# Performance work log

Hardware: AMD Instinct MI355X
Metric: run time of the kernel (lower is better)

Reference implementation:

```python
import jax, jax.numpy as jnp
import numpy as np

V, D, L, H, S, B = 30522, 768, 12, 12, 64, 128
DK = D // H
FF = 4 * D
EPS = 1e-5

def _positional_table():
    # replicates the (buggy) exponent 10000**(2*i/d) from the source
    pos = np.arange(S, dtype=np.float32)[:, None]
    i = np.arange(0, D, 2, dtype=np.float32)
    arg = pos / (10000.0 ** (2.0 * i / D))
    pe = np.zeros((S, D), dtype=np.float32)
    pe[:, 0::2] = np.sin(arg)
    pe[:, 1::2] = np.cos(arg)
    return jnp.asarray(pe)[None]  # [1,S,D]

PE = _positional_table()

def setup_inputs() -> dict:
    key = jax.random.key(0)
    ks = jax.random.split(key, 20)
    sc = 0.02
    tok_emb = jax.random.normal(ks[0], (V, D), jnp.float32) * sc
    tok_emb = tok_emb.at[0].set(0.0)  # padding_idx=0
    seg_emb = jax.random.normal(ks[1], (3, D), jnp.float32) * sc
    seg_emb = seg_emb.at[0].set(0.0)
    def w(k, shape):
        return jax.random.normal(k, shape, jnp.float32) * sc
    return {
        "x": jax.random.randint(ks[2], (B, S), 0, V),
        "segment": jax.random.randint(ks[3], (B, S), 0, 3),
        "tok_emb": tok_emb, "seg_emb": seg_emb,
        "Wq": w(ks[4], (L, D, D)), "bq": jnp.zeros((L, D)),
        "Wk": w(ks[5], (L, D, D)), "bk": jnp.zeros((L, D)),
        "Wv": w(ks[6], (L, D, D)), "bv": jnp.zeros((L, D)),
        "Wo": w(ks[7], (L, D, D)), "bo": jnp.zeros((L, D)),
        "ln_g": jnp.ones((L, D)), "ln_b": jnp.zeros((L, D)),
        "W1": w(ks[8], (L, D, FF)), "b1": jnp.zeros((L, FF)),
        "W2": w(ks[9], (L, FF, D)), "b2": jnp.zeros((L, D)),
    }

def _layernorm(x, g, b):
    mu = jnp.mean(x, -1, keepdims=True)
    var = jnp.mean(jnp.square(x - mu), -1, keepdims=True)
    return (x - mu) * jax.lax.rsqrt(var + EPS) * g + b

def reference(x, segment, tok_emb, seg_emb, Wq, bq, Wk, bk, Wv, bv, Wo, bo,
              ln_g, ln_b, W1, b1, W2, b2):
    # mask: (x>0) -> [B,1,1,S], broadcasts over query rows like the repeat in torch
    mask = (x > 0)[:, None, None, :]
    h = tok_emb[x] + seg_emb[segment] + PE  # [B,S,D]

    def layer(h, p):
        wq, bq_, wk, bk_, wv, bv_, wo, bo_, g, be, w1, b1_, w2, b2_ = p
        q = (h @ wq + bq_).reshape(B, S, H, DK).transpose(0, 2, 1, 3)
        k = (h @ wk + bk_).reshape(B, S, H, DK).transpose(0, 2, 1, 3)
        v = (h @ wv + bv_).reshape(B, S, H, DK).transpose(0, 2, 1, 3)
        scores = jnp.einsum('bhqd,bhkd->bhqk', q, k) / jnp.sqrt(jnp.float32(DK))
        scores = jnp.where(mask, scores, -1e9)
        w = jax.nn.softmax(scores, axis=-1)
        ctx = jnp.einsum('bhqk,bhkd->bhqd', w, v).transpose(0, 2, 1, 3).reshape(B, S, D)
        attn = ctx @ wo + bo_
        h1 = _layernorm(attn + h, g, be)  # shared LN params within the layer
        ff = jax.nn.gelu(h1 @ w1 + b1_, approximate=False) @ w2 + b2_
        h2 = _layernorm(h1 + ff, g, be)
        return h2, None

    params = (Wq, bq, Wk, bk, Wv, bv, Wo, bo, ln_g, ln_b, W1, b1, W2, b2)
    h, _ = jax.lax.scan(layer, h, params)
    return h
```

## Files before the change

### kernel.cpp

```cpp
#include <hip/hip_runtime.h>
#include <math.h>

typedef unsigned short u16;
typedef __bf16 bf16x8 __attribute__((ext_vector_type(8)));
typedef float f32x4 __attribute__((ext_vector_type(4)));
typedef unsigned long long u64;

__device__ __forceinline__ float bf2f(u16 u) {
    union { unsigned u32; float f; } c; c.u32 = ((unsigned)u) << 16; return c.f;
}
__device__ __forceinline__ u16 f2bf(float f) {
    unsigned u = __float_as_uint(f);
    unsigned r = u + 0x7fff + ((u >> 16) & 1);
    return (u16)(r >> 16);
}
__device__ __forceinline__ float ldmix(const void* p, u64 i, int isbf) {
    return isbf ? bf2f(((const u16*)p)[i]) : ((const float*)p)[i];
}
__device__ __forceinline__ uint4 pack8(float4 a, float4 b) {
    union { u16 h[8]; uint4 v; } u;
    u.h[0] = f2bf(a.x); u.h[1] = f2bf(a.y); u.h[2] = f2bf(a.z); u.h[3] = f2bf(a.w);
    u.h[4] = f2bf(b.x); u.h[5] = f2bf(b.y); u.h[6] = f2bf(b.z); u.h[7] = f2bf(b.w);
    return u.v;
}

__global__ void detect_kernel(const unsigned* __restrict__ tokw, int* __restrict__ flag)
{
    int i = threadIdx.x;
    unsigned w = tokw[768 + i];
    unsigned e = (w >> 7) & 0xFF;
    bool hit = (e >= 100) && (e <= 126) && ((w & 0x7FFFu) != 0);
    unsigned long long m = __ballot(hit);
    if (i == 0) flag[0] = (__popcll(m) >= 40) ? 1 : 0;
}

__global__ __launch_bounds__(256) void embed_kernel(
    const int* __restrict__ x, const int* __restrict__ seg,
    const void* __restrict__ tok, const void* __restrict__ se,
    const int* __restrict__ flagp, float* __restrict__ hF)
{
    int isbf = *flagp;
    int t = blockIdx.x;
    int pos = t & 63;
    int tokid = x[t], sgid = seg[t];
    int tid = threadIdx.x;
#pragma unroll
    for (int i = 0; i < 3; i++) {
        int d = tid + i * 256;
        int p = d >> 1;
        float freq = powf(10000.0f, (float)p * (1.0f / 192.0f));
        float arg = (float)pos / freq;
        float pe = (d & 1) ? cosf(arg) : sinf(arg);
        float v = ldmix(tok, (u64)tokid * 768 + d, isbf)
                + ldmix(se, (u64)sgid * 768 + d, isbf) + pe;
        hF[(u64)t * 768 + d] = v;
    }
}

__global__ __launch_bounds__(256) void transpose6(
    const void* __restrict__ wq, const void* __restrict__ wk,
    const void* __restrict__ wv, const void* __restrict__ wo,
    const void* __restrict__ w1, const void* __restrict__ w2,
    u16* __restrict__ out, const int* __restrict__ flagp, u64 oS, u64 oF)
{
    int isbf = *flagp;
    int id = blockIdx.x;
    const void* src; u16* dst; int R, C; u64 off;
    if (id < 2304) {
        int m = id / 576; id -= m * 576; R = 768; C = 768; off = oS;
        src = (m == 0) ? wq : (m == 1) ? wk : (m == 2) ? wv : wo;
        dst = out + (u64)m * 589824;
    } else if (id < 4608) {
        id -= 2304; R = 768; C = 3072; off = oF; src = w1; dst = out + 2359296;
    } else {
        id -= 4608; R = 3072; C = 768; off = oF; src = w2; dst = out + 4718592;
    }
    int tilesC = C >> 5;
    int tr = id / tilesC, tc = id % tilesC;
    __shared__ float tile[32][33];
    int rl = threadIdx.x >> 5, cl = threadIdx.x & 31;
#pragma unroll
    for (int i = 0; i < 4; i++)
        tile[rl + 8 * i][cl] = ldmix(src, off + (u64)(tr * 32 + rl + 8 * i) * C + tc * 32 + cl, isbf);
    __syncthreads();
#pragma unroll
    for (int i = 0; i < 4; i++)
        dst[(u64)(tc * 32 + rl + 8 * i) * R + tr * 32 + cl] = f2bf(tile[cl][rl + 8 * i]);
}

template <int MODE, int ASRC>
__global__ __launch_bounds__(256, 2) void gemm_bt(
    const void* __restrict__ Araw, const u16* __restrict__ Bt,
    const void* __restrict__ bias, u64 oB, const float* __restrict__ resid,
    float* __restrict__ outF, u16* __restrict__ outB,
    const int* __restrict__ flagp, int N, int K)
{
    constexpr int LDK = 40;
    __shared__ __align__(16) u16 sA[128 * LDK];
    __shared__ __align__(16) u16 sB[128 * LDK];
    int tid = threadIdx.x;
    int lane = tid & 63, wave = tid >> 6;
    int wr = wave >> 1, wc = wave & 1;
    int bn = blockIdx.x, bm = blockIdx.y;
    const u16* A16 = (const u16*)Araw + (u64)bm * 128 * K;
    const float* A32 = (const float*)Araw + (u64)bm * 128 * K;
    const u16* Bb = Bt + (u64)bn * 128 * K;
    int r0 = tid >> 2, c0 = (tid & 3) * 8;
    int cl = lane & 15, quad = lane >> 4;

    f32x4 acc[4][4];
    const f32x4 vz = {0.f, 0.f, 0.f, 0.f};
#pragma unroll
    for (int mi = 0; mi < 4; mi++)
#pragma unroll
        for (int ni = 0; ni < 4; ni++) acc[mi][ni] = vz;

    uint4 a0, a1;
    float4 fa0, fa1, fb0, fb1;
    if (ASRC == 0) {
        a0 = *(const uint4*)(A16 + (u64)r0 * K + c0);
        a1 = *(const uint4*)(A16 + (u64)(r0 + 64) * K + c0);
    } else {
        fa0 = *(const float4*)(A32 + (u64)r0 * K + c0);
        fa1 = *(const float4*)(A32 + (u64)r0 * K + c0 + 4);
        fb0 = *(const float4*)(A32 + (u64)(r0 + 64) * K + c0);
        fb1 = *(const float4*)(A32 + (u64)(r0 + 64) * K + c0 + 4);
    }
    uint4 g0 = *(const uint4*)(Bb + (u64)r0 * K + c0);
    uint4 g1 = *(const uint4*)(Bb + (u64)(r0 + 64) * K + c0);

    for (int k0 = 0; k0 < K; k0 += 32) {
        __syncthreads();
        if (ASRC == 0) {
            *(uint4*)(sA + r0 * LDK + c0) = a0;
            *(uint4*)(sA + (r0 + 64) * LDK + c0) = a1;
        } else {
            *(uint4*)(sA + r0 * LDK + c0) = pack8(fa0, fa1);
            *(uint4*)(sA + (r0 + 64) * LDK + c0) = pack8(fb0, fb1);
        }
        *(uint4*)(sB + r0 * LDK + c0) = g0;
        *(uint4*)(sB + (r0 + 64) * LDK + c0) = g1;
        __syncthreads();
        int kn = k0 + 32;
        if (kn < K) {
            if (ASRC == 0) {
                a0 = *(const uint4*)(A16 + (u64)r0 * K + kn + c0);
                a1 = *(const uint4*)(A16 + (u64)(r0 + 64) * K + kn + c0);
            } else {
                fa0 = *(const float4*)(A32 + (u64)r0 * K + kn + c0);
                fa1 = *(const float4*)(A32 + (u64)r0 * K + kn + c0 + 4);
                fb0 = *(const float4*)(A32 + (u64)(r0 + 64) * K + kn + c0);
                fb1 = *(const float4*)(A32 + (u64)(r0 + 64) * K + kn + c0 + 4);
            }
            g0 = *(const uint4*)(Bb + (u64)r0 * K + kn + c0);
            g1 = *(const uint4*)(Bb + (u64)(r0 + 64) * K + kn + c0);
        }
        bf16x8 af[4], bfr[4];
#pragma unroll
        for (int mi = 0; mi < 4; mi++)
            af[mi] = *(const bf16x8*)(sA + (wr * 64 + mi * 16 + cl) * LDK + quad * 8);
#pragma unroll
        for (int ni = 0; ni < 4; ni++)
            bfr[ni] = *(const bf16x8*)(sB + (wc * 64 + ni * 16 + cl) * LDK + quad * 8);
#pragma unroll
        for (int mi = 0; mi < 4; mi++)
#pragma unroll
            for (int ni = 0; ni < 4; ni++)
                acc[mi][ni] = __builtin_amdgcn_mfma_f32_16x16x32_bf16(
                    af[mi], bfr[ni], acc[mi][ni], 0, 0, 0);
    }

    int isbf = *flagp;
    int rowb = bm * 128 + wr * 64 + quad * 4;
    int colb = bn * 128 + wc * 64 + cl;
#pragma unroll
    for (int ni = 0; ni < 4; ni++) {
        int col = colb + ni * 16;
        float bv = ldmix(bias, oB + col, isbf);
#pragma unroll
        for (int mi = 0; mi < 4; mi++) {
#pragma unroll
            for (int r = 0; r < 4; r++) {
                int row = rowb + mi * 16 + r;
                float v = acc[mi][ni][r] + bv;
                if (MODE == 1) {
                    v += resid[(u64)row * N + col];
                    outF[(u64)row * N + col] = v;
                } else {
                    if (MODE == 2) v = 0.5f * v * (1.0f + erff(v * 0.70710678118654752f));
                    outB[(u64)row * N + col] = f2bf(v);
                }
            }
        }
    }
}

__global__ __launch_bounds__(256) void attn_kernel(
    const u16* __restrict__ Qg, const u16* __restrict__ Kg, const u16* __restrict__ Vg,
    const int* __restrict__ xids, u16* __restrict__ ctx)
{
    constexpr int LDA = 72;
    __shared__ __align__(16) u16 sQ[64 * LDA];
    __shared__ __align__(16) u16 sK[64 * LDA];
    __shared__ __align__(16) u16 sVt[64 * LDA];
    int tid = threadIdx.x;
    int lane = tid & 63, wave = tid >> 6;
    int b = blockIdx.x / 12, h = blockIdx.x % 12;
    {
        int r = tid >> 2, cb = (tid & 3) * 16;
        u64 gbase = ((u64)(b * 64 + r)) * 768 + h * 64 + cb;
        uint4 q0 = *(const uint4*)(Qg + gbase);
        uint4 q1 = *(const uint4*)(Qg + gbase + 8);
        uint4 k0 = *(const uint4*)(Kg + gbase);
        uint4 k1 = *(const uint4*)(Kg + gbase + 8);
        uint4 v0 = *(const uint4*)(Vg + gbase);
        uint4 v1 = *(const uint4*)(Vg + gbase + 8);
        *(uint4*)(sQ + r * LDA + cb) = q0;
        *(uint4*)(sQ + r * LDA + cb + 8) = q1;
        *(uint4*)(sK + r * LDA + cb) = k0;
        *(uint4*)(sK + r * LDA + cb + 8) = k1;
        u16 vt[16];
        *(uint4*)(vt) = v0; *(uint4*)(vt + 8) = v1;
#pragma unroll
        for (int j = 0; j < 16; j++) sVt[(cb + j) * LDA + r] = vt[j];
    }
    __syncthreads();
    int cl = lane & 15, quad = lane >> 4;

    f32x4 sc[4];
    const f32x4 vz = {0.f, 0.f, 0.f, 0.f};
#pragma unroll
    for (int ni = 0; ni < 4; ni++) sc[ni] = vz;
#pragma unroll
    for (int kt = 0; kt < 2; kt++) {
        bf16x8 a = *(const bf16x8*)(sQ + (wave * 16 + cl) * LDA + kt * 32 + quad * 8);
#pragma unroll
        for (int ni = 0; ni < 4; ni++) {
            bf16x8 bb = *(const bf16x8*)(sK + (ni * 16 + cl) * LDA + kt * 32 + quad * 8);
            sc[ni] = __builtin_amdgcn_mfma_f32_16x16x32_bf16(a, bb, sc[ni], 0, 0, 0);
        }
    }
    bool ok[4];
#pragma unroll
    for (int ni = 0; ni < 4; ni++) ok[ni] = xids[b * 64 + ni * 16 + cl] > 0;
    float p[4][4];
#pragma unroll
    for (int r = 0; r < 4; r++) {
        float m = -3.0e38f;
#pragma unroll
        for (int ni = 0; ni < 4; ni++) {
            float s = ok[ni] ? sc[ni][r] * 0.125f : -1e9f;
            p[ni][r] = s;
            m = fmaxf(m, s);
        }
#pragma unroll
        for (int off = 1; off < 16; off <<= 1) m = fmaxf(m, __shfl_xor(m, off));
        float sum = 0.f;
#pragma unroll
        for (int ni = 0; ni < 4; ni++) { float e = __expf(p[ni][r] - m); p[ni][r] = e; sum += e; }
#pragma unroll
        for (int off = 1; off < 16; off <<= 1) sum += __shfl_xor(sum, off);
        float inv = 1.0f / sum;
#pragma unroll
        for (int ni = 0; ni < 4; ni++) p[ni][r] *= inv;
    }
    __syncthreads();
#pragma unroll
    for (int ni = 0; ni < 4; ni++)
#pragma unroll
        for (int r = 0; r < 4; r++)
            sQ[(wave * 16 + quad * 4 + r) * LDA + ni * 16 + cl] = f2bf(p[ni][r]);
    __syncthreads();
    f32x4 o[4];
#pragma unroll
    for (int ni = 0; ni < 4; ni++) o[ni] = vz;
#pragma unroll
    for (int kt = 0; kt < 2; kt++) {
        bf16x8 a = *(const bf16x8*)(sQ + (wave * 16 + cl) * LDA + kt * 32 + quad * 8);
#pragma unroll
        for (int ni = 0; ni < 4; ni++) {
            bf16x8 bb = *(const bf16x8*)(sVt + (ni * 16 + cl) * LDA + kt * 32 + quad * 8);
            o[ni] = __builtin_amdgcn_mfma_f32_16x16x32_bf16(a, bb, o[ni], 0, 0, 0);
        }
    }
#pragma unroll
    for (int ni = 0; ni < 4; ni++)
#pragma unroll
        for (int r = 0; r < 4; r++)
            ctx[((u64)(b * 64 + wave * 16 + quad * 4 + r)) * 768 + h * 64 + ni * 16 + cl] =
                f2bf(o[ni][r]);
}

__global__ __launch_bounds__(256) void ln_kernel(
    const float* __restrict__ X, const void* __restrict__ g, const void* __restrict__ bta,
    const int* __restrict__ flagp, float* __restrict__ outF, void* __restrict__ outD,
    int isfinal, u64 oB)
{
    int isbf = *flagp;
    int t = blockIdx.x;
    const float* xr = X + (u64)t * 768;
    int tid = threadIdx.x;
    float v0 = xr[tid], v1 = xr[tid + 256], v2 = xr[tid + 512];
    float s = v0 + v1 + v2;
    float sq = v0 * v0 + v1 * v1 + v2 * v2;
#pragma unroll
    for (int off = 1; off < 64; off <<= 1) { s += __shfl_xor(s, off); sq += __shfl_xor(sq, off); }
    __shared__ float red[8];
    int lane = tid & 63, wave = tid >> 6;
    if (lane == 0) { red[wave] = s; red[4 + wave] = sq; }
    __syncthreads();
    s = red[0] + red[1] + red[2] + red[3];
    sq = red[4] + red[5] + red[6] + red[7];
    float mu = s * (1.0f / 768.0f);
    float var = sq * (1.0f / 768.0f) - mu * mu;
    float rs = rsqrtf(var + 1e-5f);
    float* of = outF + (u64)t * 768;
#pragma unroll
    for (int i = 0; i < 3; i++) {
        int c = tid + i * 256;
        float v = (i == 0) ? v0 : (i == 1) ? v1 : v2;
        float y = (v - mu) * rs * ldmix(g, oB + c, isbf) + ldmix(bta, oB + c, isbf);
        of[c] = y;
        if (isfinal) {
            if (isbf) ((u16*)outD)[(u64)t * 768 + c] = f2bf(y);
            else      ((float*)outD)[(u64)t * 768 + c] = y;
        }
    }
}

extern "C" void kernel_launch(void* const* d_in, const int* in_sizes, int n_in,
                              void* d_out, int out_size, void* d_ws, size_t ws_size,
                              hipStream_t stream)
{
    const int* x    = (const int*)d_in[0];
    const int* seg  = (const int*)d_in[1];
    const void* tok = d_in[2];
    const void* sege= d_in[3];
    const void* Wq  = d_in[4];
    const void* bq  = d_in[5];
    const void* Wk  = d_in[6];
    const void* bk  = d_in[7];
    const void* Wv  = d_in[8];
    const void* bv  = d_in[9];
    const void* Wo  = d_in[10];
    const void* bo  = d_in[11];
    const void* lng = d_in[12];
    const void* lnb = d_in[13];
    const void* W1  = d_in[14];
    const void* b1  = d_in[15];
    const void* W2  = d_in[16];
    const void* b2  = d_in[17];

    const u64 ND = 8192ull * 768ull;
    char* p = (char*)d_ws;
    auto alloc = [&](size_t bytes) { char* q = p; p += (bytes + 255) & ~(size_t)255; return q; };
    int*   flag = (int*)alloc(256);
    float* hF   = (float*)alloc(ND * 4);
    float* xF   = (float*)alloc(ND * 4);
    u16*   qB   = (u16*)alloc(ND * 2);
    u16*   kB   = (u16*)alloc(ND * 2);
    u16*   vB   = (u16*)alloc(ND * 2);
    u16*   ctxB = (u16*)alloc(ND * 2);
    u16*   ffB  = qB;
    u16*   Wt   = (u16*)alloc(7077888ull * 2);

    detect_kernel<<<1, 64, 0, stream>>>((const unsigned*)tok, flag);
    embed_kernel<<<8192, 256, 0, stream>>>(x, seg, tok, sege, flag, hF);

    dim3 g768(6, 64), g3072(24, 64);
    for (int l = 0; l < 12; l++) {
        const u64 oS = (u64)l * 589824ull, oF = (u64)l * 2359296ull;
        const u64 oB = (u64)l * 768ull, oB1 = (u64)l * 3072ull;
        transpose6<<<6912, 256, 0, stream>>>(Wq, Wk, Wv, Wo, W1, W2, Wt, flag, oS, oF);
        gemm_bt<0, 1><<<g768, 256, 0, stream>>>(hF, Wt,              bq, oB, nullptr, nullptr, qB, flag, 768, 768);
        gemm_bt<0, 1><<<g768, 256, 0, stream>>>(hF, Wt + 589824,     bk, oB, nullptr, nullptr, kB, flag, 768, 768);
        gemm_bt<0, 1><<<g768, 256, 0, stream>>>(hF, Wt + 1179648,    bv, oB, nullptr, nullptr, vB, flag, 768, 768);
        attn_kernel<<<1536, 256, 0, stream>>>(qB, kB, vB, x, ctxB);
        gemm_bt<1, 0><<<g768, 256, 0, stream>>>(ctxB, Wt + 1769472,  bo, oB, hF, xF, nullptr, flag, 768, 768);
        ln_kernel<<<8192, 256, 0, stream>>>(xF, lng, lnb, flag, xF, nullptr, 0, oB);
        gemm_bt<2, 1><<<g3072, 256, 0, stream>>>(xF, Wt + 2359296,   b1, oB1, nullptr, nullptr, ffB, flag, 3072, 768);
        gemm_bt<1, 0><<<g768, 256, 0, stream>>>(ffB, Wt + 4718592,   b2, oB, xF, xF, nullptr, flag, 768, 3072);
        ln_kernel<<<8192, 256, 0, stream>>>(xF, lng, lnb, flag, hF,
                                            (l == 11) ? d_out : nullptr,
                                            (l == 11) ? 1 : 0, oB);
    }
}
```

Baseline: 4.153 ms.

## Fuse QKV GEMMs, feed bf16 activations, and load GEMM tiles via global_load_lds

Merges the three Q/K/V projections into one GEMM over a contiguous 2304-column transposed weight block, picking the bias per column segment, and has attention read from the packed QKV buffer. Embedding and layernorm kernels now also write bf16 copies of their activations, so the GEMMs read bf16 A directly instead of converting fp32 on load. The GEMM tile staging switches from register-staged loads to direct global-to-LDS loads with an unpadded LDS layout. The extra bf16 writes add memory traffic, the unpadded layout may cause LDS bank conflicts, and the single LDS buffer now needs a different read/sync ordering.

Measured after the change: 3.561 ms. 1.17x faster.

```diff
diff --git a/kernel.cpp b/kernel.cpp
--- a/kernel.cpp
+++ b/kernel.cpp
@@ -17,11 +17,10 @@
 __device__ __forceinline__ float ldmix(const void* p, u64 i, int isbf) {
     return isbf ? bf2f(((const u16*)p)[i]) : ((const float*)p)[i];
 }
-__device__ __forceinline__ uint4 pack8(float4 a, float4 b) {
-    union { u16 h[8]; uint4 v; } u;
-    u.h[0] = f2bf(a.x); u.h[1] = f2bf(a.y); u.h[2] = f2bf(a.z); u.h[3] = f2bf(a.w);
-    u.h[4] = f2bf(b.x); u.h[5] = f2bf(b.y); u.h[6] = f2bf(b.z); u.h[7] = f2bf(b.w);
-    return u.v;
+__device__ __forceinline__ void gll16(const u16* g, u16* l) {
+    __builtin_amdgcn_global_load_lds(
+        (const __attribute__((address_space(1))) void*)g,
+        (__attribute__((address_space(3))) void*)l, 16, 0, 0);
 }
 
 __global__ void detect_kernel(const unsigned* __restrict__ tokw, int* __restrict__ flag)
@@ -37,7 +36,7 @@
 __global__ __launch_bounds__(256) void embed_kernel(
     const int* __restrict__ x, const int* __restrict__ seg,
     const void* __restrict__ tok, const void* __restrict__ se,
-    const int* __restrict__ flagp, float* __restrict__ hF)
+    const int* __restrict__ flagp, float* __restrict__ hF, u16* __restrict__ hB)
 {
     int isbf = *flagp;
     int t = blockIdx.x;
@@ -54,6 +53,7 @@
         float v = ldmix(tok, (u64)tokid * 768 + d, isbf)
                 + ldmix(se, (u64)sgid * 768 + d, isbf) + pe;
         hF[(u64)t * 768 + d] = v;
+        hB[(u64)t * 768 + d] = f2bf(v);
     }
 }
 
@@ -88,24 +88,32 @@
         dst[(u64)(tc * 32 + rl + 8 * i) * R + tr * 32 + cl] = f2bf(tile[cl][rl + 8 * i]);
 }
 
-template <int MODE, int ASRC>
+template <int MODE>
 __global__ __launch_bounds__(256, 2) void gemm_bt(
-    const void* __restrict__ Araw, const u16* __restrict__ Bt,
-    const void* __restrict__ bias, u64 oB, const float* __restrict__ resid,
+    const u16* __restrict__ A, const u16* __restrict__ Bt,
+    const void* __restrict__ bA, const void* __restrict__ bB,
+    const void* __restrict__ bC, u64 oB, const float* __restrict__ resid,
     float* __restrict__ outF, u16* __restrict__ outB,
     const int* __restrict__ flagp, int N, int K)
 {
-    constexpr int LDK = 40;
-    __shared__ __align__(16) u16 sA[128 * LDK];
-    __shared__ __align__(16) u16 sB[128 * LDK];
+    __shared__ __align__(16) u16 sA[128 * 32];
+    __shared__ __align__(16) u16 sB[128 * 32];
     int tid = threadIdx.x;
     int lane = tid & 63, wave = tid >> 6;
     int wr = wave >> 1, wc = wave & 1;
     int bn = blockIdx.x, bm = blockIdx.y;
-    const u16* A16 = (const u16*)Araw + (u64)bm * 128 * K;
-    const float* A32 = (const float*)Araw + (u64)bm * 128 * K;
+    const u16* Ab = A + (u64)bm * 128 * K;
     const u16* Bb = Bt + (u64)bn * 128 * K;
-    int r0 = tid >> 2, c0 = (tid & 3) * 8;
+    int srow = tid >> 2;
+    int scol = (tid & 3) * 8;
+    u16* sAw0 = sA + wave * 512;
+    u16* sAw1 = sA + 2048 + wave * 512;
+    u16* sBw0 = sB + wave * 512;
+    u16* sBw1 = sB + 2048 + wave * 512;
+    const u16* Ar0 = Ab + (u64)srow * K + scol;
+    const u16* Ar1 = Ab + (u64)(srow + 64) * K + scol;
+    const u16* Br0 = Bb + (u64)srow * K + scol;
+    const u16* Br1 = Bb + (u64)(srow + 64) * K + scol;
     int cl = lane & 15, quad = lane >> 4;
 
     f32x4 acc[4][4];
@@ -115,53 +123,24 @@
 #pragma unroll
         for (int ni = 0; ni < 4; ni++) acc[mi][ni] = vz;
 
-    uint4 a0, a1;
-    float4 fa0, fa1, fb0, fb1;
-    if (ASRC == 0) {
-        a0 = *(const uint4*)(A16 + (u64)r0 * K + c0);
-        a1 = *(const uint4*)(A16 + (u64)(r0 + 64) * K + c0);
-    } else {
-        fa0 = *(const float4*)(A32 + (u64)r0 * K + c0);
-        fa1 = *(const float4*)(A32 + (u64)r0 * K + c0 + 4);
-        fb0 = *(const float4*)(A32 + (u64)(r0 + 64) * K + c0);
-        fb1 = *(const float4*)(A32 + (u64)(r0 + 64) * K + c0 + 4);
-    }
-    uint4 g0 = *(const uint4*)(Bb + (u64)r0 * K + c0);
-    uint4 g1 = *(const uint4*)(Bb + (u64)(r0 + 64) * K + c0);
+    gll16(Ar0, sAw0); gll16(Ar1, sAw1);
+    gll16(Br0, sBw0); gll16(Br1, sBw1);
 
     for (int k0 = 0; k0 < K; k0 += 32) {
         __syncthreads();
-        if (ASRC == 0) {
-            *(uint4*)(sA + r0 * LDK + c0) = a0;
-            *(uint4*)(sA + (r0 + 64) * LDK + c0) = a1;
-        } else {
-            *(uint4*)(sA + r0 * LDK + c0) = pack8(fa0, fa1);
-            *(uint4*)(sA + (r0 + 64) * LDK + c0) = pack8(fb0, fb1);
-        }
-        *(uint4*)(sB + r0 * LDK + c0) = g0;
-        *(uint4*)(sB + (r0 + 64) * LDK + c0) = g1;
+        bf16x8 af[4], bfr[4];
+#pragma unroll
+        for (int mi = 0; mi < 4; mi++)
+            af[mi] = *(const bf16x8*)(sA + (wr * 64 + mi * 16 + cl) * 32 + quad * 8);
+#pragma unroll
+        for (int ni = 0; ni < 4; ni++)
+            bfr[ni] = *(const bf16x8*)(sB + (wc * 64 + ni * 16 + cl) * 32 + quad * 8);
         __syncthreads();
         int kn = k0 + 32;
         if (kn < K) {
-            if (ASRC == 0) {
-                a0 = *(const uint4*)(A16 + (u64)r0 * K + kn + c0);
-                a1 = *(const uint4*)(A16 + (u64)(r0 + 64) * K + kn + c0);
-            } else {
-                fa0 = *(const float4*)(A32 + (u64)r0 * K + kn + c0);
-                fa1 = *(const float4*)(A32 + (u64)r0 * K + kn + c0 + 4);
-                fb0 = *(const float4*)(A32 + (u64)(r0 + 64) * K + kn + c0);
-                fb1 = *(const float4*)(A32 + (u64)(r0 + 64) * K + kn + c0 + 4);
-            }
-            g0 = *(const uint4*)(Bb + (u64)r0 * K + kn + c0);
-            g1 = *(const uint4*)(Bb + (u64)(r0 + 64) * K + kn + c0);
-        }
-        bf16x8 af[4], bfr[4];
-#pragma unroll
-        for (int mi = 0; mi < 4; mi++)
-            af[mi] = *(const bf16x8*)(sA + (wr * 64 + mi * 16 + cl) * LDK + quad * 8);
-#pragma unroll
-        for (int ni = 0; ni < 4; ni++)
-            bfr[ni] = *(const bf16x8*)(sB + (wc * 64 + ni * 16 + cl) * LDK + quad * 8);
+            gll16(Ar0 + kn, sAw0); gll16(Ar1 + kn, sAw1);
+            gll16(Br0 + kn, sBw0); gll16(Br1 + kn, sBw1);
+        }
 #pragma unroll
         for (int mi = 0; mi < 4; mi++)
 #pragma unroll
@@ -173,10 +152,17 @@
     int isbf = *flagp;
     int rowb = bm * 128 + wr * 64 + quad * 4;
     int colb = bn * 128 + wc * 64 + cl;
+    const void* bp = bA;
+    int csub = 0;
+    if (MODE == 3) {
+        int ms = bn / 6;
+        bp = (ms == 0) ? bA : (ms == 1) ? bB : bC;
+        csub = ms * 768;
+    }
 #pragma unroll
     for (int ni = 0; ni < 4; ni++) {
         int col = colb + ni * 16;
-        float bv = ldmix(bias, oB + col, isbf);
+        float bv = ldmix(bp, oB + (u64)(col - csub), isbf);
 #pragma unroll
         for (int mi = 0; mi < 4; mi++) {
 #pragma unroll
@@ -196,8 +182,7 @@
 }
 
 __global__ __launch_bounds__(256) void attn_kernel(
-    const u16* __restrict__ Qg, const u16* __restrict__ Kg, const u16* __restrict__ Vg,
-    const int* __restrict__ xids, u16* __restrict__ ctx)
+    const u16* __restrict__ QKV, const int* __restrict__ xids, u16* __restrict__ ctx)
 {
     constexpr int LDA = 72;
     __shared__ __align__(16) u16 sQ[64 * LDA];
@@ -208,13 +193,13 @@
     int b = blockIdx.x / 12, h = blockIdx.x % 12;
     {
         int r = tid >> 2, cb = (tid & 3) * 16;
-        u64 gbase = ((u64)(b * 64 + r)) * 768 + h * 64 + cb;
-        uint4 q0 = *(const uint4*)(Qg + gbase);
-        uint4 q1 = *(const uint4*)(Qg + gbase + 8);
-        uint4 k0 = *(const uint4*)(Kg + gbase);
-        uint4 k1 = *(const uint4*)(Kg + gbase + 8);
-        uint4 v0 = *(const uint4*)(Vg + gbase);
-        uint4 v1 = *(const uint4*)(Vg + gbase + 8);
+        u64 gbase = ((u64)(b * 64 + r)) * 2304 + h * 64 + cb;
+        uint4 q0 = *(const uint4*)(QKV + gbase);
+        uint4 q1 = *(const uint4*)(QKV + gbase + 8);
+        uint4 k0 = *(const uint4*)(QKV + gbase + 768);
+        uint4 k1 = *(const uint4*)(QKV + gbase + 776);
+        uint4 v0 = *(const uint4*)(QKV + gbase + 1536);
+        uint4 v1 = *(const uint4*)(QKV + gbase + 1544);
         *(uint4*)(sQ + r * LDA + cb) = q0;
         *(uint4*)(sQ + r * LDA + cb + 8) = q1;
         *(uint4*)(sK + r * LDA + cb) = k0;
@@ -293,8 +278,8 @@
 
 __global__ __launch_bounds__(256) void ln_kernel(
     const float* __restrict__ X, const void* __restrict__ g, const void* __restrict__ bta,
-    const int* __restrict__ flagp, float* __restrict__ outF, void* __restrict__ outD,
-    int isfinal, u64 oB)
+    const int* __restrict__ flagp, float* __restrict__ outF, u16* __restrict__ outH,
+    void* __restrict__ outD, int isfinal, u64 oB)
 {
     int isbf = *flagp;
     int t = blockIdx.x;
@@ -321,6 +306,7 @@
         float v = (i == 0) ? v0 : (i == 1) ? v1 : v2;
         float y = (v - mu) * rs * ldmix(g, oB + c, isbf) + ldmix(bta, oB + c, isbf);
         of[c] = y;
+        outH[(u64)t * 768 + c] = f2bf(y);
         if (isfinal) {
             if (isbf) ((u16*)outD)[(u64)t * 768 + c] = f2bf(y);
             else      ((float*)outD)[(u64)t * 768 + c] = y;
@@ -357,30 +343,32 @@
     int*   flag = (int*)alloc(256);
     float* hF   = (float*)alloc(ND * 4);
     float* xF   = (float*)alloc(ND * 4);
-    u16*   qB   = (u16*)alloc(ND * 2);
-    u16*   kB   = (u16*)alloc(ND * 2);
-    u16*   vB   = (u16*)alloc(ND * 2);
+    u16*   hB   = (u16*)alloc(ND * 2);
+    u16*   xB   = (u16*)alloc(ND * 2);
+    u16*   qkvB = (u16*)alloc(ND * 3 * 2);
     u16*   ctxB = (u16*)alloc(ND * 2);
-    u16*   ffB  = qB;
+    u16*   ffB  = qkvB;
     u16*   Wt   = (u16*)alloc(7077888ull * 2);
 
     detect_kernel<<<1, 64, 0, stream>>>((const unsigned*)tok, flag);
-    embed_kernel<<<8192, 256, 0, stream>>>(x, seg, tok, sege, flag, hF);
-
-    dim3 g768(6, 64), g3072(24, 64);
+    embed_kernel<<<8192, 256, 0, stream>>>(x, seg, tok, sege, flag, hF, hB);
+
+    dim3 g768(6, 64), g2304(18, 64), g3072(24, 64);
     for (int l = 0; l < 12; l++) {
         const u64 oS = (u64)l * 589824ull, oF = (u64)l * 2359296ull;
         const u64 oB = (u64)l * 768ull, oB1 = (u64)l * 3072ull;
         transpose6<<<6912, 256, 0, stream>>>(Wq, Wk, Wv, Wo, W1, W2, Wt, flag, oS, oF);
-        gemm_bt<0, 1><<<g768, 256, 0, stream>>>(hF, Wt,              bq, oB, nullptr, nullptr, qB, flag, 768, 768);
-        gemm_bt<0, 1><<<g768, 256, 0, stream>>>(hF, Wt + 589824,     bk, oB, nullptr, nullptr, kB, flag, 768, 768);
-        gemm_bt<0, 1><<<g768, 256, 0, stream>>>(hF, Wt + 1179648,    bv, oB, nullptr, nullptr, vB, flag, 768, 768);
-        attn_kernel<<<1536, 256, 0, stream>>>(qB, kB, vB, x, ctxB);
-        gemm_bt<1, 0><<<g768, 256, 0, stream>>>(ctxB, Wt + 1769472,  bo, oB, hF, xF, nullptr, flag, 768, 768);
-        ln_kernel<<<8192, 256, 0, stream>>>(xF, lng, lnb, flag, xF, nullptr, 0, oB);
-        gemm_bt<2, 1><<<g3072, 256, 0, stream>>>(xF, Wt + 2359296,   b1, oB1, nullptr, nullptr, ffB, flag, 3072, 768);
-        gemm_bt<1, 0><<<g768, 256, 0, stream>>>(ffB, Wt + 4718592,   b2, oB, xF, xF, nullptr, flag, 768, 3072);
-        ln_kernel<<<8192, 256, 0, stream>>>(xF, lng, lnb, flag, hF,
+        gemm_bt<3><<<g2304, 256, 0, stream>>>(hB, Wt, bq, bk, bv, oB,
+                                              nullptr, nullptr, qkvB, flag, 2304, 768);
+        attn_kernel<<<1536, 256, 0, stream>>>(qkvB, x, ctxB);
+        gemm_bt<1><<<g768, 256, 0, stream>>>(ctxB, Wt + 1769472, bo, nullptr, nullptr, oB,
+                                             hF, xF, nullptr, flag, 768, 768);
+        ln_kernel<<<8192, 256, 0, stream>>>(xF, lng, lnb, flag, xF, xB, nullptr, 0, oB);
+        gemm_bt<2><<<g3072, 256, 0, stream>>>(xB, Wt + 2359296, b1, nullptr, nullptr, oB1,
+                                              nullptr, nullptr, ffB, flag, 3072, 768);
+        gemm_bt<1><<<g768, 256, 0, stream>>>(ffB, Wt + 4718592, b2, nullptr, nullptr, oB,
+                                             xF, xF, nullptr, flag, 768, 3072);
+        ln_kernel<<<8192, 256, 0, stream>>>(xF, lng, lnb, flag, hF, hB,
                                             (l == 11) ? d_out : nullptr,
                                             (l == 11) ? 1 : 0, oB);
     }
```
